# Performance work log

Measured on AMD Instinct MI355X. Metric: run time of the kernel, lower is better.

The kernel has to match this reference:

```python
import jax, jax.numpy as jnp
import numpy as np

# dims
B, S, E = 32, 2048, 512          # batch, seq_length, emb_size
N, P, K = 256, 16, 16            # new_seq_len, sample_num, sub_seq_len
STRIDE = 8                       # ceil(S / N)
PAD = 4                          # ceil((STRIDE*(N-1) + K - S) / 2)


def setup_inputs() -> dict:
    key = jax.random.key(0)
    ks = jax.random.split(key, 6)
    return {
        "x": jax.random.normal(ks[0], (B, S, E), jnp.float32),
        "conv_w": jax.random.normal(ks[1], (E, E, K), jnp.float32) / np.float32(np.sqrt(E * K)),
        "conv_b": jax.random.normal(ks[2], (E,), jnp.float32) * 0.01,
        "lin_w": jax.random.normal(ks[3], (2, E), jnp.float32) / np.float32(np.sqrt(E)),
        "lin_b": jax.random.normal(ks[4], (2,), jnp.float32) * 0.01,
        "width_bias": jnp.asarray(0.5 * np.log(5.0 / 3.0), jnp.float32),  # log(sqrt(5/3))
    }


def reference(x, conv_w, conv_b, lin_w, lin_b, width_bias):
    # --- proj: Conv1d over sequence, [B,S,E] -> [B,N,E] ---
    xc = jnp.transpose(x, (0, 2, 1))  # [B,E,S]
    y = jax.lax.conv_general_dilated(
        xc, conv_w, (STRIDE,), [(PAD, PAD)],
        dimension_numbers=("NCH", "OIH", "NCH"),
    ) + conv_b[None, :, None]  # [B,E,N]
    y = jnp.transpose(y, (0, 2, 1))  # [B,N,E]

    # --- offset prediction: ReLU -> Linear(E, 2) ---
    off = jax.nn.relu(y) @ lin_w.T + lin_b  # [B,N,2]

    # --- SubSeqCoder.decode (weights = (1,1), width_bias added to last channel) ---
    anchor = (0.5 + jnp.arange(N, dtype=x.dtype)) / N  # [N]
    poi = 1.0 / N
    dx = jnp.tanh(off[:, :, 0]) * poi
    dw = jax.nn.relu(jnp.tanh(off[:, :, 1] + width_bias)) * poi
    x0 = jnp.clip(anchor[None, :] + dx - dw, 0.0, 1.0)  # box start, [B,N]
    x1 = jnp.clip(anchor[None, :] + dx + dw, 0.0, 1.0)  # box end

    # --- sample: linear interpolate (align_corners=True) from 2 -> P points ---
    t = jnp.linspace(0.0, 1.0, P, dtype=x.dtype)  # [P]
    gx = x0[:, :, None] * (1.0 - t) + x1[:, :, None] * t  # [B,N,P] in [0,1]

    # --- grid_sample nearest, padding_mode='border', align_corners=False ---
    gx = 2.0 * gx - 1.0  # normalized grid coord
    ix = ((gx + 1.0) * S - 1.0) * 0.5  # unnormalize (align_corners=False)
    idx = jnp.clip(jnp.round(ix).astype(jnp.int32), 0, S - 1)  # [B,N,P], round half-even matches nearbyint
    vals = jnp.take_along_axis(x, idx.reshape(B, N * P, 1), axis=1)  # [B,N*P,E]
    # output already in [B, N, P, E] layout (== torch permute(0,2,3,1))
    return vals.reshape(B, N, P, E)
```

## Files before the change

### kernel.cpp

```cpp
#include <hip/hip_runtime.h>
#include <cmath>

#define BATCH 32
#define SEQ   2048
#define EMB   512
#define NOUT  256
#define PS    16
#define KW    16
#define JTOT  8192
#define KCL   288

#define MT 128
#define NT 128
#define KS 32

#define GLDS16(g_, l_) __builtin_amdgcn_global_load_lds(                      \
    (__attribute__((address_space(1))) const void*)(g_),                      \
    (__attribute__((address_space(3))) void*)(l_), 16, 0, 0)

__device__ __forceinline__ float xla_tanhf(float x) {
#pragma clang fp contract(off)
    float ax = fabsf(x);
    float xc = x;
    if (xc < -7.90531110763549805f) xc = -7.90531110763549805f;
    if (xc >  7.90531110763549805f) xc =  7.90531110763549805f;
    float x2 = xc * xc;
    float p = __builtin_fmaf(x2, -2.76076847742355e-16f, 2.00018790482477e-13f);
    p = __builtin_fmaf(x2, p, -8.60467152213735e-11f);
    p = __builtin_fmaf(x2, p,  5.12229709037114e-08f);
    p = __builtin_fmaf(x2, p,  1.48572235717979e-05f);
    p = __builtin_fmaf(x2, p,  6.37261928875436e-04f);
    p = __builtin_fmaf(x2, p,  4.89352455891786e-03f);
    float num = xc * p;
    float q = __builtin_fmaf(x2, 1.19825839466702e-06f, 1.18534705686654e-04f);
    q = __builtin_fmaf(x2, q, 2.26843463243900e-03f);
    q = __builtin_fmaf(x2, q, 4.89352518554385e-03f);
    float r = num / q;
    return (ax < 0.0004f) ? x : r;
}

__global__ __launch_bounds__(256) void k_transpose_w(const float* __restrict__ w,
                                                     float* __restrict__ wT) {
    int t = blockIdx.x * 256 + threadIdx.x;
    int o = t & 511;
    int i = (t >> 9) & 511;
    int k = t >> 18;
    wT[t] = w[(size_t)o * 8192 + i * 16 + k];
}

__global__ __launch_bounds__(256, 1) void k_conv(const float* __restrict__ x,
                                                 const float* __restrict__ wT,
                                                 const float* __restrict__ cb,
                                                 float* __restrict__ y) {
#pragma clang fp contract(off)
    __shared__ __align__(16) float sA[2][KS][MT];
    __shared__ __align__(16) float sB[2][KS][NT];

    int bn0 = blockIdx.x << 7;
    int b   = bn0 >> 8;
    int n0  = bn0 & 255;
    int o0  = blockIdx.y << 7;

    int tid  = threadIdx.x;
    int tm   = tid & 15;
    int tn   = tid >> 4;
    int lane = tid & 63;
    int wv   = tid >> 6;

    float ys[8][8], pk[8][8];
#pragma unroll
    for (int mi = 0; mi < 8; ++mi)
#pragma unroll
        for (int ni = 0; ni < 8; ++ni) { ys[mi][ni] = 0.0f; pk[mi][ni] = 0.0f; }

    const float* xb = x + (size_t)b * SEQ * EMB;

    float4 ra[4];

#define LOAD_A(js_)                                                            \
    {                                                                          \
        int k_  = (js_) >> 4;                                                  \
        int i0_ = ((js_) & 15) << 5;                                           \
        _Pragma("unroll")                                                      \
        for (int r = 0; r < 4; ++r) {                                          \
            int q  = tid + (r << 8);                                           \
            int m  = q >> 3;                                                   \
            int c4 = (q & 7) << 2;                                             \
            int s  = ((n0 + m) << 3) - 4 + k_;                                 \
            ra[r] = make_float4(0.f, 0.f, 0.f, 0.f);                           \
            if (s >= 0 && s < SEQ)                                             \
                ra[r] = *(const float4*)(xb + ((size_t)s << 9) + i0_ + c4);    \
        }                                                                      \
    }

#define WRITE_A(bf_)                                                           \
    {                                                                          \
        _Pragma("unroll")                                                      \
        for (int r = 0; r < 4; ++r) {                                          \
            int q  = tid + (r << 8);                                           \
            int m  = q >> 3;                                                   \
            int c4 = (q & 7) << 2;                                             \
            sA[bf_][c4 + 0][m] = ra[r].x;                                      \
            sA[bf_][c4 + 1][m] = ra[r].y;                                      \
            sA[bf_][c4 + 2][m] = ra[r].z;                                      \
            sA[bf_][c4 + 3][m] = ra[r].w;                                      \
        }                                                                      \
    }

#define STAGE_B(js_, bf_)                                                      \
    {                                                                          \
        _Pragma("unroll")                                                      \
        for (int t = 0; t < 4; ++t) {                                          \
            int kkb = (wv << 3) + (t << 1);                                    \
            const float* gsrc = wT + (((size_t)((js_) << 5) + kkb + (lane >> 5)) << 9) \
                                   + o0 + ((lane & 31) << 2);                  \
            GLDS16(gsrc, &sB[bf_][kkb][0]);                                    \
        }                                                                      \
    }

    LOAD_A(0);
    WRITE_A(0);
    STAGE_B(0, 0);
    __syncthreads();

    for (int js = 0; js < 256; ++js) {
        int cur = js & 1;
        if (js < 255) {
            LOAD_A(js + 1);
            STAGE_B(js + 1, cur ^ 1);
        }

#pragma unroll
        for (int kk = 0; kk < KS; ++kk) {
            float4 a0 = *(const float4*)&sA[cur][kk][tm << 2];
            float4 a1 = *(const float4*)&sA[cur][kk][64 + (tm << 2)];
            float4 b0 = *(const float4*)&sB[cur][kk][tn << 2];
            float4 b1 = *(const float4*)&sB[cur][kk][64 + (tn << 2)];
            float av[8] = {a0.x, a0.y, a0.z, a0.w, a1.x, a1.y, a1.z, a1.w};
            float bv[8] = {b0.x, b0.y, b0.z, b0.w, b1.x, b1.y, b1.z, b1.w};
#pragma unroll
            for (int mi = 0; mi < 8; ++mi)
#pragma unroll
                for (int ni = 0; ni < 8; ++ni)
                    pk[mi][ni] = __builtin_fmaf(av[mi], bv[ni], pk[mi][ni]);
        }
        if ((js % 9) == 8 || js == 255) {
#pragma unroll
            for (int mi = 0; mi < 8; ++mi)
#pragma unroll
                for (int ni = 0; ni < 8; ++ni) {
                    ys[mi][ni] = ys[mi][ni] + pk[mi][ni];
                    pk[mi][ni] = 0.0f;
                }
        }
        if (js < 255) WRITE_A(cur ^ 1);
        __syncthreads();
    }

#pragma unroll
    for (int mi = 0; mi < 8; ++mi) {
        int m = (mi < 4) ? ((tm << 2) + mi) : (64 + (tm << 2) + mi - 4);
        int n = n0 + m;
        float* dst = y + (((size_t)(b << 8) + n) << 9) + o0;
#pragma unroll
        for (int ni = 0; ni < 8; ++ni) {
            int oo = (ni < 4) ? ((tn << 2) + ni) : (64 + (tn << 2) + ni - 4);
            dst[oo] = ys[mi][ni] + cb[o0 + oo];
        }
    }
#undef LOAD_A
#undef WRITE_A
#undef STAGE_B
}

__global__ __launch_bounds__(256) void k_decode(const float* __restrict__ y,
                                               const float* __restrict__ lw,
                                               const float* __restrict__ lb,
                                               const float* __restrict__ wb,
                                               int* __restrict__ idx) {
#pragma clang fp contract(off)
    int bn = blockIdx.x * 256 + threadIdx.x;
    if (bn >= BATCH * NOUT) return;
    const float* yy = y + ((size_t)bn << 9);

    float s0, s1;
    {
        float p0 = 0.0f, p1 = 0.0f;
        for (int e = 0; e < KCL; ++e) {
            float v = yy[e];
            float r = v > 0.0f ? v : 0.0f;
            p0 = __builtin_fmaf(r, lw[e],       p0);
            p1 = __builtin_fmaf(r, lw[EMB + e], p1);
        }
        s0 = p0; s1 = p1;
    }
    {
        float p0 = 0.0f, p1 = 0.0f;
        for (int e = KCL; e < EMB; ++e) {
            float v = yy[e];
            float r = v > 0.0f ? v : 0.0f;
            p0 = __builtin_fmaf(r, lw[e],       p0);
            p1 = __builtin_fmaf(r, lw[EMB + e], p1);
        }
        s0 = s0 + p0; s1 = s1 + p1;
    }
    float off0 = s0 + lb[0];
    float off1 = s1 + lb[1];

    int n = bn & (NOUT - 1);
    float anchor = (0.5f + (float)n) / 256.0f;
    float dx  = xla_tanhf(off0) * 0.00390625f;
    float a1  = off1 + wb[0];
    float tww = xla_tanhf(a1);
    float rwv = tww > 0.0f ? tww : 0.0f;
    float dwv = rwv * 0.00390625f;
    float adx = anchor + dx;
    float x0 = adx - dwv; x0 = x0 < 0.0f ? 0.0f : (x0 > 1.0f ? 1.0f : x0);
    float x1 = adx + dwv; x1 = x1 < 0.0f ? 0.0f : (x1 > 1.0f ? 1.0f : x1);

    const float delta = 1.0f / 15.0f;
#pragma unroll
    for (int p = 0; p < PS; ++p) {
        float t  = (float)p * delta;
        float om = 1.0f - t;
        float gs = x0 * om + x1 * t;
        float gxn = 2.0f * gs - 1.0f;
        float gp1 = gxn + 1.0f;
        float ixx = (gp1 * 2048.0f - 1.0f) * 0.5f;
        float rr = rintf(ixx);
        int id = (int)rr;
        id = id < 0 ? 0 : (id > SEQ - 1 ? SEQ - 1 : id);
        idx[bn * PS + p] = id;
    }
}

__global__ __launch_bounds__(128) void k_gather(const float* __restrict__ x,
                                                const int* __restrict__ idx,
                                                float* __restrict__ out) {
    int g = blockIdx.x;
    int b = g >> 12;
    int sidx = idx[g];
    const float4* src = (const float4*)(x + (((size_t)b * SEQ + sidx) << 9));
    float4* dst = (float4*)(out + ((size_t)g << 9));
    dst[threadIdx.x] = src[threadIdx.x];
}

extern "C" void kernel_launch(void* const* d_in, const int* in_sizes, int n_in,
                              void* d_out, int out_size, void* d_ws, size_t ws_size,
                              hipStream_t stream) {
    const float* x      = (const float*)d_in[0];
    const float* conv_w = (const float*)d_in[1];
    const float* conv_b = (const float*)d_in[2];
    const float* lin_w  = (const float*)d_in[3];
    const float* lin_b  = (const float*)d_in[4];
    const float* wbias  = (const float*)d_in[5];
    float* out = (float*)d_out;

    float* wT  = (float*)d_out;
    float* y   = (float*)((char*)d_out + (size_t)16777216);
    int*   idx = (int*)d_ws;

    hipLaunchKernelGGL(k_transpose_w, dim3(16384), dim3(256), 0, stream, conv_w, wT);
    hipLaunchKernelGGL(k_conv,        dim3(64, 4), dim3(256), 0, stream, x, wT, conv_b, y);
    hipLaunchKernelGGL(k_decode,      dim3(32),    dim3(256), 0, stream, y, lin_w, lin_b, wbias, idx);
    hipLaunchKernelGGL(k_gather,      dim3(BATCH * NOUT * PS), dim3(128), 0, stream, x, idx, out);
}
```

Before: 1.186 ms.

## Shrink conv GEMM tiles to 64x64 with one row per thread

The conv GEMM tile drops from 128x128 to 64x64, so the grid grows from 256 to 1024 blocks, with two blocks per CU allowed by the launch bounds. Each thread now owns one output row (its lane) and a 16-wide column strip (per wave), instead of an 8x8 register micro-tile. The aim is more resident waves to hide load latency and better fill of the CUs. The cost is lower reuse: more LDS reads per FMA and more global traffic per output, because inputs are reused less across the smaller tiles.

```diff
diff --git a/kernel.cpp b/kernel.cpp
--- a/kernel.cpp
+++ b/kernel.cpp
@@ -9,10 +9,7 @@
 #define KW    16
 #define JTOT  8192
 #define KCL   288
-
-#define MT 128
-#define NT 128
-#define KS 32
+#define KS    32
 
 #define GLDS16(g_, l_) __builtin_amdgcn_global_load_lds(                      \
     (__attribute__((address_space(1))) const void*)(g_),                      \
@@ -48,72 +45,65 @@
     wT[t] = w[(size_t)o * 8192 + i * 16 + k];
 }
 
-__global__ __launch_bounds__(256, 1) void k_conv(const float* __restrict__ x,
+__global__ __launch_bounds__(256, 2) void k_conv(const float* __restrict__ x,
                                                  const float* __restrict__ wT,
                                                  const float* __restrict__ cb,
                                                  float* __restrict__ y) {
 #pragma clang fp contract(off)
-    __shared__ __align__(16) float sA[2][KS][MT];
-    __shared__ __align__(16) float sB[2][KS][NT];
-
-    int bn0 = blockIdx.x << 7;
+    __shared__ __align__(16) float sA[2][KS][64];
+    __shared__ __align__(16) float sB[2][KS][64];
+
+    int bn0 = blockIdx.x << 6;
     int b   = bn0 >> 8;
     int n0  = bn0 & 255;
-    int o0  = blockIdx.y << 7;
+    int o0  = blockIdx.y << 6;
 
     int tid  = threadIdx.x;
-    int tm   = tid & 15;
-    int tn   = tid >> 4;
     int lane = tid & 63;
-    int wv   = tid >> 6;
-
-    float ys[8][8], pk[8][8];
-#pragma unroll
-    for (int mi = 0; mi < 8; ++mi)
-#pragma unroll
-        for (int ni = 0; ni < 8; ++ni) { ys[mi][ni] = 0.0f; pk[mi][ni] = 0.0f; }
+    int w    = tid >> 6;
+    int wo0  = w << 4;
+
+    float ys[16], pk[16];
+#pragma unroll
+    for (int ni = 0; ni < 16; ++ni) { ys[ni] = 0.0f; pk[ni] = 0.0f; }
 
     const float* xb = x + (size_t)b * SEQ * EMB;
 
-    float4 ra[4];
+    float4 ra[2];
 
 #define LOAD_A(js_)                                                            \
     {                                                                          \
         int k_  = (js_) >> 4;                                                  \
         int i0_ = ((js_) & 15) << 5;                                           \
+        int s_  = ((n0 + lane) << 3) - 4 + k_;                                 \
         _Pragma("unroll")                                                      \
-        for (int r = 0; r < 4; ++r) {                                          \
-            int q  = tid + (r << 8);                                           \
-            int m  = q >> 3;                                                   \
-            int c4 = (q & 7) << 2;                                             \
-            int s  = ((n0 + m) << 3) - 4 + k_;                                 \
+        for (int r = 0; r < 2; ++r) {                                          \
+            int c4 = (w << 2) + (r << 4);                                      \
             ra[r] = make_float4(0.f, 0.f, 0.f, 0.f);                           \
-            if (s >= 0 && s < SEQ)                                             \
-                ra[r] = *(const float4*)(xb + ((size_t)s << 9) + i0_ + c4);    \
+            if (s_ >= 0 && s_ < SEQ)                                           \
+                ra[r] = *(const float4*)(xb + ((size_t)s_ << 9) + i0_ + c4);   \
         }                                                                      \
     }
 
 #define WRITE_A(bf_)                                                           \
     {                                                                          \
         _Pragma("unroll")                                                      \
-        for (int r = 0; r < 4; ++r) {                                          \
-            int q  = tid + (r << 8);                                           \
-            int m  = q >> 3;                                                   \
-            int c4 = (q & 7) << 2;                                             \
-            sA[bf_][c4 + 0][m] = ra[r].x;                                      \
-            sA[bf_][c4 + 1][m] = ra[r].y;                                      \
-            sA[bf_][c4 + 2][m] = ra[r].z;                                      \
-            sA[bf_][c4 + 3][m] = ra[r].w;                                      \
+        for (int r = 0; r < 2; ++r) {                                          \
+            int c4 = (w << 2) + (r << 4);                                      \
+            sA[bf_][c4 + 0][lane] = ra[r].x;                                   \
+            sA[bf_][c4 + 1][lane] = ra[r].y;                                   \
+            sA[bf_][c4 + 2][lane] = ra[r].z;                                   \
+            sA[bf_][c4 + 3][lane] = ra[r].w;                                   \
         }                                                                      \
     }
 
 #define STAGE_B(js_, bf_)                                                      \
     {                                                                          \
         _Pragma("unroll")                                                      \
-        for (int t = 0; t < 4; ++t) {                                          \
-            int kkb = (wv << 3) + (t << 1);                                    \
-            const float* gsrc = wT + (((size_t)((js_) << 5) + kkb + (lane >> 5)) << 9) \
-                                   + o0 + ((lane & 31) << 2);                  \
+        for (int t2 = 0; t2 < 2; ++t2) {                                       \
+            int kkb = (w << 3) + (t2 << 2);                                    \
+            const float* gsrc = wT + (((size_t)((js_) << 5) + kkb + (lane >> 4)) << 9) \
+                                   + o0 + ((lane & 15) << 2);                  \
             GLDS16(gsrc, &sB[bf_][kkb][0]);                                    \
         }                                                                      \
     }
@@ -132,41 +122,35 @@
 
 #pragma unroll
         for (int kk = 0; kk < KS; ++kk) {
-            float4 a0 = *(const float4*)&sA[cur][kk][tm << 2];
-            float4 a1 = *(const float4*)&sA[cur][kk][64 + (tm << 2)];
-            float4 b0 = *(const float4*)&sB[cur][kk][tn << 2];
-            float4 b1 = *(const float4*)&sB[cur][kk][64 + (tn << 2)];
-            float av[8] = {a0.x, a0.y, a0.z, a0.w, a1.x, a1.y, a1.z, a1.w};
-            float bv[8] = {b0.x, b0.y, b0.z, b0.w, b1.x, b1.y, b1.z, b1.w};
-#pragma unroll
-            for (int mi = 0; mi < 8; ++mi)
-#pragma unroll
-                for (int ni = 0; ni < 8; ++ni)
-                    pk[mi][ni] = __builtin_fmaf(av[mi], bv[ni], pk[mi][ni]);
+            float a = sA[cur][kk][lane];
+            float4 b0 = *(const float4*)&sB[cur][kk][wo0];
+            float4 b1 = *(const float4*)&sB[cur][kk][wo0 + 4];
+            float4 b2 = *(const float4*)&sB[cur][kk][wo0 + 8];
+            float4 b3 = *(const float4*)&sB[cur][kk][wo0 + 12];
+            float bv[16] = {b0.x, b0.y, b0.z, b0.w, b1.x, b1.y, b1.z, b1.w,
+                            b2.x, b2.y, b2.z, b2.w, b3.x, b3.y, b3.z, b3.w};
+#pragma unroll
+            for (int ni = 0; ni < 16; ++ni)
+                pk[ni] = __builtin_fmaf(a, bv[ni], pk[ni]);
         }
         if ((js % 9) == 8 || js == 255) {
 #pragma unroll
-            for (int mi = 0; mi < 8; ++mi)
-#pragma unroll
-                for (int ni = 0; ni < 8; ++ni) {
-                    ys[mi][ni] = ys[mi][ni] + pk[mi][ni];
-                    pk[mi][ni] = 0.0f;
-                }
+            for (int ni = 0; ni < 16; ++ni) {
+                ys[ni] = ys[ni] + pk[ni];
+                pk[ni] = 0.0f;
+            }
         }
         if (js < 255) WRITE_A(cur ^ 1);
         __syncthreads();
     }
 
-#pragma unroll
-    for (int mi = 0; mi < 8; ++mi) {
-        int m = (mi < 4) ? ((tm << 2) + mi) : (64 + (tm << 2) + mi - 4);
-        int n = n0 + m;
-        float* dst = y + (((size_t)(b << 8) + n) << 9) + o0;
-#pragma unroll
-        for (int ni = 0; ni < 8; ++ni) {
-            int oo = (ni < 4) ? ((tn << 2) + ni) : (64 + (tn << 2) + ni - 4);
-            dst[oo] = ys[mi][ni] + cb[o0 + oo];
-        }
+    {
+        int n = n0 + lane;
+        float* dst = y + (((size_t)(b << 8) + n) << 9) + o0 + wo0;
+        const float* cbp = cb + o0 + wo0;
+#pragma unroll
+        for (int ni = 0; ni < 16; ++ni)
+            dst[ni] = ys[ni] + cbp[ni];
     }
 #undef LOAD_A
 #undef WRITE_A
@@ -261,7 +245,7 @@
     int*   idx = (int*)d_ws;
 
     hipLaunchKernelGGL(k_transpose_w, dim3(16384), dim3(256), 0, stream, conv_w, wT);
-    hipLaunchKernelGGL(k_conv,        dim3(64, 4), dim3(256), 0, stream, x, wT, conv_b, y);
+    hipLaunchKernelGGL(k_conv,        dim3(128, 8), dim3(256), 0, stream, x, wT, conv_b, y);
     hipLaunchKernelGGL(k_decode,      dim3(32),    dim3(256), 0, stream, y, lin_w, lin_b, wbias, idx);
     hipLaunchKernelGGL(k_gather,      dim3(BATCH * NOUT * PS), dim3(128), 0, stream, x, idx, out);
 }
```

Measured after the change: 1.476 ms. 1.25x slower.
